# Performance work log

Measured on AMD Instinct MI355X. Metric: run time of the kernel, lower is better.

The kernel has to match this reference:

```python
import jax, jax.numpy as jnp
import numpy as np

P = 20000          # plan nodes (queries)
H = 128            # hidden_dim_plan
DIMS = {"table": (100000, 96), "pred": (400000, 160), "agg": (60000, 64), "join": (80000, 64)}
BN_EPS = 1e-5


def setup_inputs() -> dict:
    key = jax.random.key(0)
    ks = iter(jax.random.split(key, 32))
    inp = {}
    for t, (n, d) in DIMS.items():
        inp[f"feat_{t}"] = jax.random.normal(next(ks), (n, d), dtype=jnp.float32)
        inp[f"idx_{t}"] = jax.random.randint(next(ks), (n,), 0, P)
        # per-type encoder: Linear(d, H) (stored as [d, H])
        inp[f"W_{t}"] = jax.random.normal(next(ks), (d, H), dtype=jnp.float32) * 0.02
        inp[f"b_{t}"] = jnp.zeros((H,), jnp.float32)
    # est head: BatchNorm1d(4H) -> Linear(4H,H)+ReLU -> Linear(H,H)+ReLU -> Linear(H,1)
    inp["bn_gamma"] = jnp.ones((4 * H,), jnp.float32)
    inp["bn_beta"] = jnp.zeros((4 * H,), jnp.float32)
    inp["W1"] = jax.random.normal(next(ks), (4 * H, H), dtype=jnp.float32) * 0.02
    inp["b1"] = jnp.zeros((H,), jnp.float32)
    inp["W2"] = jax.random.normal(next(ks), (H, H), dtype=jnp.float32) * 0.02
    inp["b2"] = jnp.zeros((H,), jnp.float32)
    inp["W3"] = jax.random.normal(next(ks), (H, 1), dtype=jnp.float32) * 0.02
    inp["b3"] = jnp.zeros((1,), jnp.float32)
    inp["num_plan"] = P
    return inp


def _seg_mean(x, idx, num_seg):
    # DGL mean pooling: mean over incoming edges, 0 for nodes with no edges
    s = jax.ops.segment_sum(x, idx, num_segments=num_seg)
    c = jax.ops.segment_sum(jnp.ones((x.shape[0], 1), x.dtype), idx, num_segments=num_seg)
    return s / jnp.maximum(c, 1.0)


def _forward(feats, idxs, params, num_plan):
    pooled = []
    for t in ("table", "pred", "agg", "join"):
        enc = jax.nn.relu(feats[t] @ params[f"W_{t}"] + params[f"b_{t}"])  # [N_t, H]
        pooled.append(_seg_mean(enc, idxs[t], num_plan))                    # [P, H]
    x = jnp.concatenate(pooled, axis=1)  # [P, 4H]
    # BatchNorm1d (training mode: batch statistics, biased variance)
    mu = jnp.mean(x, axis=0)
    var = jnp.mean(jnp.square(x - mu), axis=0)
    x = (x - mu) * jax.lax.rsqrt(var + BN_EPS) * params["bn_gamma"] + params["bn_beta"]
    x = jax.nn.relu(x @ params["W1"] + params["b1"])
    x = jax.nn.relu(x @ params["W2"] + params["b2"])
    return x @ params["W3"] + params["b3"]  # [P, 1]


def reference(feat_table, feat_pred, feat_agg, feat_join,
              W_table, b_table, W_pred, b_pred, W_agg, b_agg, W_join, b_join,
              bn_gamma, bn_beta, W1, b1, W2, b2, W3, b3,
              idx_table, idx_pred, idx_agg, idx_join, num_plan):
    feats = {"table": feat_table, "pred": feat_pred, "agg": feat_agg, "join": feat_join}
    idxs = {"table": idx_table, "pred": idx_pred, "agg": idx_agg, "join": idx_join}
    params = dict(W_table=W_table, b_table=b_table, W_pred=W_pred, b_pred=b_pred,
                  W_agg=W_agg, b_agg=b_agg, W_join=W_join, b_join=b_join,
                  bn_gamma=bn_gamma, bn_beta=bn_beta, W1=W1, b1=b1, W2=W2, b2=b2, W3=W3, b3=b3)
    return _forward(feats, idxs, params, num_plan)
```

## Files before the change

### kernel.cpp

```cpp
#include <hip/hip_runtime.h>
#include <cstdint>


constexpr int P_N = 20000;
constexpr int HD  = 128;

typedef __attribute__((ext_vector_type(8))) short  short8v;
typedef __attribute__((ext_vector_type(4))) float  float4v;
typedef __attribute__((ext_vector_type(8))) float  float8v;
typedef __attribute__((ext_vector_type(8))) __bf16 bf16x8;

__device__ inline ushort f2bf(float f) {
    uint32_t u = __builtin_bit_cast(uint32_t, f);
    u += 0x7fffu + ((u >> 16) & 1u);
    return (ushort)(u >> 16);
}
__device__ inline short8v cvt8v(float4 a, float4 b) {
    float8v f = {a.x, a.y, a.z, a.w, b.x, b.y, b.z, b.w};
    bf16x8 h = __builtin_convertvector(f, bf16x8);
    return __builtin_bit_cast(short8v, h);
}
__device__ inline float4v mfma16(short8v a, short8v b, float4v c) {
    return __builtin_amdgcn_mfma_f32_16x16x32_bf16(a, b, c, 0, 0, 0);
}

__global__ void k_count_all(const int* __restrict__ i0, const int* __restrict__ i1,
                            const int* __restrict__ i2, const int* __restrict__ i3,
                            int n0, int n1, int n2, int n3, int* __restrict__ counts) {
    int i = blockIdx.x * blockDim.x + threadIdx.x;
    const int n01 = n0 + n1, n012 = n0 + n1 + n2, tot = n012 + n3;
    if (i >= tot) return;
    int tp, li; const int* p;
    if (i < n0)        { tp = 0; li = i;        p = i0; }
    else if (i < n01)  { tp = 1; li = i - n0;   p = i1; }
    else if (i < n012) { tp = 2; li = i - n01;  p = i2; }
    else               { tp = 3; li = i - n012; p = i3; }
    atomicAdd(&counts[tp * P_N + p[li]], 1);
}

__global__ void k_scan(int* __restrict__ counts_all, int* __restrict__ off_all,
                       int* __restrict__ cur_all, float* __restrict__ invc,
                       int* l0, int* l1, int* l2, int* l3,
                       int* s0, int* s1, int* s2, int* s3,
                       int n0, int n1, int n2, int n3) {
    const int type = blockIdx.x;
    int* counts = counts_all + type * P_N;
    int* offs   = off_all   + type * P_N;
    int* curs   = cur_all   + type * P_N;
    float* ic   = invc      + type * P_N;
    const int T = 256;
    const int CH = (P_N + T - 1) / T;
    int t = threadIdx.x;
    __shared__ int sums[T];
    __shared__ int pref[T];
    int local = 0;
    int p0 = t * CH;
    for (int i = 0; i < CH; ++i) {
        int p = p0 + i;
        if (p < P_N) local += counts[p];
    }
    sums[t] = local;
    __syncthreads();
    if (t == 0) {
        int run = 0;
        for (int j = 0; j < T; ++j) { pref[j] = run; run += sums[j]; }
    }
    __syncthreads();
    int run = pref[t];
    for (int i = 0; i < CH; ++i) {
        int p = p0 + i;
        if (p < P_N) {
            int c = counts[p];
            offs[p] = run; curs[p] = run; run += c;
            ic[p] = 1.f / (float)max(c, 1);
        }
    }
    int N; int *lp, *sp;
    if (type == 0)      { N = n0; lp = l0; sp = s0; }
    else if (type == 1) { N = n1; lp = l1; sp = s1; }
    else if (type == 2) { N = n2; lp = l2; sp = s2; }
    else                { N = n3; lp = l3; sp = s3; }
    if (t < 160) { lp[N + t] = 0; sp[N + t] = -1; }
}

__global__ void k_fill_all(const int* __restrict__ i0, const int* __restrict__ i1,
                           const int* __restrict__ i2, const int* __restrict__ i3,
                           int n0, int n1, int n2, int n3, int* __restrict__ cur_all,
                           int* l0, int* l1, int* l2, int* l3,
                           int* s0, int* s1, int* s2, int* s3) {
    int i = blockIdx.x * blockDim.x + threadIdx.x;
    const int n01 = n0 + n1, n012 = n0 + n1 + n2, tot = n012 + n3;
    if (i >= tot) return;
    int tp, li; const int* p; int *lst, *spl;
    if (i < n0)        { tp = 0; li = i;        p = i0; lst = l0; spl = s0; }
    else if (i < n01)  { tp = 1; li = i - n0;   p = i1; lst = l1; spl = s1; }
    else if (i < n012) { tp = 2; li = i - n01;  p = i2; lst = l2; spl = s2; }
    else               { tp = 3; li = i - n012; p = i3; lst = l3; spl = s3; }
    int pl = p[li];
    int pos = atomicAdd(&cur_all[tp * P_N + pl], 1);
    lst[pos] = li;
    spl[pos] = pl;
}

__global__ void k_prepw_all(const float* s0, const float* s1, const float* s2,
                            const float* s3, const float* s4, const float* s5,
                            ushort* d0, ushort* d1, ushort* d2, ushort* d3,
                            ushort* d4, ushort* d5) {
    int i = blockIdx.x * blockDim.x + threadIdx.x;
    const float* s; ushort* d; int Dv, li;
    if (i < 12288)       { s = s0; d = d0; Dv = 96;  li = i; }
    else if (i < 32768)  { s = s1; d = d1; Dv = 160; li = i - 12288; }
    else if (i < 40960)  { s = s2; d = d2; Dv = 64;  li = i - 32768; }
    else if (i < 49152)  { s = s3; d = d3; Dv = 64;  li = i - 40960; }
    else if (i < 114688) { s = s4; d = d4; Dv = 512; li = i - 49152; }
    else if (i < 131072) { s = s5; d = d5; Dv = 128; li = i - 114688; }
    else return;
    int n = li / Dv, k = li - n * Dv;
    d[li] = f2bf(s[k * HD + n]);
}

__device__ __forceinline__ void reduce_group(float (*Cs)[132], const int* plans,
                                             float* __restrict__ x, int toff, int pbase) {
    const int t = threadIdx.x;
    const int col = t & 127, half = t >> 7;
    int curp = -2; float s = 0.f;
    #pragma unroll 8
    for (int r = 0; r < 32; ++r) {
        int p = plans[pbase + half * 32 + r];
        float v = Cs[half * 32 + r][col];
        if (p != curp) {
            if (curp >= 0) atomicAdd(&x[(size_t)curp * 512 + toff + col], s);
            s = 0.f; curp = p;
        }
        if (p >= 0) s += v;
    }
    if (curp >= 0) atomicAdd(&x[(size_t)curp * 512 + toff + col], s);
}

template<int D>
__device__ __forceinline__ void enc_body(
    const float* __restrict__ feat, const ushort* __restrict__ WT,
    const float* __restrict__ bias, const int* __restrict__ list,
    const int* __restrict__ splan, float* __restrict__ x, int toff, int tile,
    float (*Cs)[132], int* plans)
{
    constexpr int NKS = D / 32;
    const int t = threadIdx.x;
    const int w = t >> 6, lane = t & 63;
    const int lq = lane >> 4, lr = lane & 15;
    const int m0 = tile * 128;

    if (t < 128) plans[t] = splan[m0 + t];
    const int l0v = list[m0 + w * 16 + lr];
    const int l1v = list[m0 + 64 + w * 16 + lr];

    const float* a0p = feat + (size_t)l0v * D + lq * 8;
    const float* a1p = feat + (size_t)l1v * D + lq * 8;

    float4 s0[2 * NKS], s1[2 * NKS];
    #pragma unroll
    for (int ks = 0; ks < NKS; ++ks) {
        s0[2 * ks]     = *(const float4*)(a0p + ks * 32);
        s0[2 * ks + 1] = *(const float4*)(a0p + ks * 32 + 4);
    }
    #pragma unroll
    for (int ks = 0; ks < NKS; ++ks) {
        s1[2 * ks]     = *(const float4*)(a1p + ks * 32);
        s1[2 * ks + 1] = *(const float4*)(a1p + ks * 32 + 4);
    }
    short8v a0[NKS], a1[NKS];
    #pragma unroll
    for (int ks = 0; ks < NKS; ++ks) a0[ks] = cvt8v(s0[2 * ks], s0[2 * ks + 1]);
    #pragma unroll
    for (int ks = 0; ks < NKS; ++ks) a1[ks] = cvt8v(s1[2 * ks], s1[2 * ks + 1]);

    float bv[8];
    #pragma unroll
    for (int nf = 0; nf < 8; ++nf) bv[nf] = bias[nf * 16 + lr];

    float4v acc0[8], acc1[8];
    #pragma unroll
    for (int nf = 0; nf < 8; ++nf) {
        acc0[nf] = (float4v){0.f, 0.f, 0.f, 0.f};
        acc1[nf] = (float4v){0.f, 0.f, 0.f, 0.f};
    }

    const ushort* wp = WT + lr * D + lq * 8;
    short8v bcur[8];
    #pragma unroll
    for (int nf = 0; nf < 8; ++nf) bcur[nf] = *(const short8v*)(wp + nf * 16 * D);
    #pragma unroll
    for (int ks = 0; ks < NKS; ++ks) {
        short8v bnxt[8];
        if (ks + 1 < NKS) {
            #pragma unroll
            for (int nf = 0; nf < 8; ++nf)
                bnxt[nf] = *(const short8v*)(wp + nf * 16 * D + (ks + 1) * 32);
        }
        #pragma unroll
        for (int nf = 0; nf < 8; ++nf) acc0[nf] = mfma16(a0[ks], bcur[nf], acc0[nf]);
        #pragma unroll
        for (int nf = 0; nf < 8; ++nf) acc1[nf] = mfma16(a1[ks], bcur[nf], acc1[nf]);
        if (ks + 1 < NKS) {
            #pragma unroll
            for (int nf = 0; nf < 8; ++nf) bcur[nf] = bnxt[nf];
        }
    }

    #pragma unroll
    for (int nf = 0; nf < 8; ++nf) {
        #pragma unroll
        for (int j = 0; j < 4; ++j)
            Cs[w * 16 + lq * 4 + j][nf * 16 + lr] = fmaxf(acc0[nf][j] + bv[nf], 0.f);
    }
    __syncthreads();
    reduce_group(Cs, plans, x, toff, 0);
    __syncthreads();
    #pragma unroll
    for (int nf = 0; nf < 8; ++nf) {
        #pragma unroll
        for (int j = 0; j < 4; ++j)
            Cs[w * 16 + lq * 4 + j][nf * 16 + lr] = fmaxf(acc1[nf][j] + bv[nf], 0.f);
    }
    __syncthreads();
    reduce_group(Cs, plans, x, toff, 64);
}

__global__ __launch_bounds__(256, 2) void k_enc_all(
    const float* f0, const float* f1, const float* f2, const float* f3,
    const ushort* w0, const ushort* w1, const ushort* w2, const ushort* w3,
    const float* b0, const float* b1, const float* b2, const float* b3,
    const int* l0, const int* l1, const int* l2, const int* l3,
    const int* s0, const int* s1, const int* s2, const int* s3,
    float* x, int ntp, int ntt, int nta)
{
    __shared__ float Cs[64][132];
    __shared__ int plans[128];
    int bid = blockIdx.x;
    if (bid < ntp) { enc_body<160>(f1, w1, b1, l1, s1, x, 128, bid, Cs, plans); return; }
    bid -= ntp;
    if (bid < ntt) { enc_body<96>(f0, w0, b0, l0, s0, x, 0, bid, Cs, plans); return; }
    bid -= ntt;
    if (bid < nta) { enc_body<64>(f2, w2, b2, l2, s2, x, 256, bid, Cs, plans); return; }
    bid -= nta;
    enc_body<64>(f3, w3, b3, l3, s3, x, 384, bid, Cs, plans);
}

__global__ __launch_bounds__(512) void k_bnstats(const float* __restrict__ x,
                                                 const float* __restrict__ invc,
                                                 float* __restrict__ bnsum) {
    const int t = threadIdx.x;
    const int r0 = blockIdx.x * 40;
    const int r1 = min(r0 + 40, P_N);
    const float* ic = invc + (t >> 7) * P_N;
    float s = 0.f, q = 0.f;
    for (int r = r0; r < r1; ++r) {
        float v = x[(size_t)r * 512 + t] * ic[r];
        s += v; q += v * v;
    }
    atomicAdd(&bnsum[t], s);
    atomicAdd(&bnsum[512 + t], q);
}

__global__ __launch_bounds__(512) void k_bnfinal(const float* __restrict__ bnsum,
                                                 const float* __restrict__ gamma, const float* __restrict__ beta,
                                                 float* __restrict__ scale, float* __restrict__ shiftv) {
    const int t = threadIdx.x;
    const float invn = 1.f / (float)P_N;
    float mu  = bnsum[t] * invn;
    float var = bnsum[512 + t] * invn - mu * mu;
    float rstd = rsqrtf(fmaxf(var, 0.f) + 1e-5f);
    float sc = gamma[t] * rstd;
    scale[t]  = sc;
    shiftv[t] = beta[t] - mu * sc;
}

__global__ __launch_bounds__(256) void k_head(
    const float* __restrict__ x, const float* __restrict__ invc,
    const float* __restrict__ scale, const float* __restrict__ shiftv,
    const ushort* __restrict__ WT1, const float* __restrict__ b1,
    const ushort* __restrict__ WT2, const float* __restrict__ b2,
    const float* __restrict__ W3, const float* __restrict__ b3,
    float* __restrict__ out)
{
    __shared__ float h[2][16][132];
    __shared__ float red[2][32];
    const int t = threadIdx.x;
    const int w = t >> 6, lane = t & 63;
    const int lq = lane >> 4, lr = lane & 15;
    const int wr = w >> 1, wc = w & 1;
    const int p0 = blockIdx.x * 32;
    const int row = p0 + wr * 16 + lr;
    const float* xr = x + (size_t)row * 512;

    float4v acc[4];
    #pragma unroll
    for (int nf = 0; nf < 4; ++nf) acc[nf] = (float4v){0.f, 0.f, 0.f, 0.f};

    #pragma unroll
    for (int kc = 0; kc < 4; ++kc) {
        const float ic = invc[kc * P_N + row];
        float4 st[8];
        #pragma unroll
        for (int k2 = 0; k2 < 4; ++k2) {
            const int k0 = kc * 128 + k2 * 32 + lq * 8;
            st[2 * k2]     = *(const float4*)(xr + k0);
            st[2 * k2 + 1] = *(const float4*)(xr + k0 + 4);
        }
        short8v a[4];
        #pragma unroll
        for (int k2 = 0; k2 < 4; ++k2) {
            const int k0 = kc * 128 + k2 * 32 + lq * 8;
            float4 sc0 = *(const float4*)(scale + k0);
            float4 sc1 = *(const float4*)(scale + k0 + 4);
            float4 sh0 = *(const float4*)(shiftv + k0);
            float4 sh1 = *(const float4*)(shiftv + k0 + 4);
            float4 v0, v1;
            v0.x = st[2*k2].x   * ic * sc0.x + sh0.x;
            v0.y = st[2*k2].y   * ic * sc0.y + sh0.y;
            v0.z = st[2*k2].z   * ic * sc0.z + sh0.z;
            v0.w = st[2*k2].w   * ic * sc0.w + sh0.w;
            v1.x = st[2*k2+1].x * ic * sc1.x + sh1.x;
            v1.y = st[2*k2+1].y * ic * sc1.y + sh1.y;
            v1.z = st[2*k2+1].z * ic * sc1.z + sh1.z;
            v1.w = st[2*k2+1].w * ic * sc1.w + sh1.w;
            a[k2] = cvt8v(v0, v1);
        }
        #pragma unroll
        for (int k2 = 0; k2 < 4; ++k2) {
            const int ks = kc * 4 + k2;
            #pragma unroll
            for (int nf = 0; nf < 4; ++nf) {
                short8v b = *(const short8v*)(WT1 + (size_t)(wc * 64 + nf * 16 + lr) * 512 + ks * 32 + lq * 8);
                acc[nf] = mfma16(a[k2], b, acc[nf]);
            }
        }
    }
    #pragma unroll
    for (int nf = 0; nf < 4; ++nf) {
        const int c = wc * 64 + nf * 16 + lr;
        const float bvv = b1[c];
        #pragma unroll
        for (int j = 0; j < 4; ++j)
            h[wr][lq * 4 + j][c] = fmaxf(acc[nf][j] + bvv, 0.f);
    }
    __syncthreads();

    short8v a2[4];
    #pragma unroll
    for (int ks = 0; ks < 4; ++ks) {
        const float* hp = &h[wr][lr][ks * 32 + lq * 8];
        a2[ks] = cvt8v(*(const float4*)hp, *(const float4*)(hp + 4));
    }
    float4v acc2[4];
    #pragma unroll
    for (int nf = 0; nf < 4; ++nf) acc2[nf] = (float4v){0.f, 0.f, 0.f, 0.f};
    #pragma unroll
    for (int ks = 0; ks < 4; ++ks) {
        #pragma unroll
        for (int nf = 0; nf < 4; ++nf) {
            short8v b = *(const short8v*)(WT2 + (wc * 64 + nf * 16 + lr) * 128 + ks * 32 + lq * 8);
            acc2[nf] = mfma16(a2[ks], b, acc2[nf]);
        }
    }

    float s0 = 0.f, s1 = 0.f, s2 = 0.f, s3 = 0.f;
    #pragma unroll
    for (int nf = 0; nf < 4; ++nf) {
        const int c = wc * 64 + nf * 16 + lr;
        const float w3v = W3[c];
        const float bvv = b2[c];
        s0 += fmaxf(acc2[nf][0] + bvv, 0.f) * w3v;
        s1 += fmaxf(acc2[nf][1] + bvv, 0.f) * w3v;
        s2 += fmaxf(acc2[nf][2] + bvv, 0.f) * w3v;
        s3 += fmaxf(acc2[nf][3] + bvv, 0.f) * w3v;
    }
    #pragma unroll
    for (int o = 1; o < 16; o <<= 1) {
        s0 += __shfl_xor(s0, o);
        s1 += __shfl_xor(s1, o);
        s2 += __shfl_xor(s2, o);
        s3 += __shfl_xor(s3, o);
    }
    if (lr == 0) {
        red[wc][wr * 16 + lq * 4 + 0] = s0;
        red[wc][wr * 16 + lq * 4 + 1] = s1;
        red[wc][wr * 16 + lq * 4 + 2] = s2;
        red[wc][wr * 16 + lq * 4 + 3] = s3;
    }
    __syncthreads();
    if (t < 32) out[p0 + t] = red[0][t] + red[1][t] + b3[0];
}

extern "C" void kernel_launch(void* const* d_in, const int* in_sizes, int n_in,
                              void* d_out, int out_size, void* d_ws, size_t ws_size,
                              hipStream_t stream)
{
    const float* feats[4] = {(const float*)d_in[0], (const float*)d_in[4], (const float*)d_in[8],  (const float*)d_in[12]};
    const int*   idxs[4]  = {(const int*)d_in[1],   (const int*)d_in[5],   (const int*)d_in[9],   (const int*)d_in[13]};
    const float* Ws[4]    = {(const float*)d_in[2], (const float*)d_in[6], (const float*)d_in[10], (const float*)d_in[14]};
    const float* bs[4]    = {(const float*)d_in[3], (const float*)d_in[7], (const float*)d_in[11], (const float*)d_in[15]};
    const float* gamma = (const float*)d_in[16];
    const float* beta  = (const float*)d_in[17];
    const float* W1 = (const float*)d_in[18]; const float* b1 = (const float*)d_in[19];
    const float* W2 = (const float*)d_in[20]; const float* b2 = (const float*)d_in[21];
    const float* W3 = (const float*)d_in[22]; const float* b3 = (const float*)d_in[23];
    int Ns[4] = {in_sizes[1], in_sizes[5], in_sizes[9], in_sizes[13]};

    char* ws = (char*)d_ws;
    int* counts = (int*)(ws + 0);
    int* offs   = (int*)(ws + 320000);
    int* curs   = (int*)(ws + 640000);
    int* lists[4];
    lists[0] = (int*)(ws + 960000);
    lists[1] = (int*)(ws + 1360640);
    lists[2] = (int*)(ws + 2961280);
    lists[3] = (int*)(ws + 3201920);
    int* splans[4];
    splans[0] = (int*)(ws + 3522560);
    splans[1] = (int*)(ws + 3923200);
    splans[2] = (int*)(ws + 5523840);
    splans[3] = (int*)(ws + 5764480);
    ushort* WTs[4];
    WTs[0] = (ushort*)(ws + 6085120);
    WTs[1] = (ushort*)(ws + 6109696);
    WTs[2] = (ushort*)(ws + 6150656);
    WTs[3] = (ushort*)(ws + 6167040);
    float* invc   = (float*)(ws + 6183424);
    float* x      = (float*)(ws + 6503424);
    float* bnsum  = (float*)(ws + 47463424);
    float* scale  = (float*)(ws + 47467520);
    float* shiftv = (float*)(ws + 47469568);
    ushort* WT1   = (ushort*)(ws + 640000);
    ushort* WT2   = (ushort*)(ws + 771072);

    hipMemsetAsync(counts, 0, 4 * P_N * sizeof(int), stream);
    hipMemsetAsync(bnsum, 0, 1024 * sizeof(float), stream);
    hipMemsetAsync(x, 0, (size_t)P_N * 512 * sizeof(float), stream);

    const int tot = Ns[0] + Ns[1] + Ns[2] + Ns[3];
    k_count_all<<<(tot + 255) / 256, 256, 0, stream>>>(
        idxs[0], idxs[1], idxs[2], idxs[3], Ns[0], Ns[1], Ns[2], Ns[3], counts);
    k_scan<<<4, 256, 0, stream>>>(counts, offs, curs, invc,
        lists[0], lists[1], lists[2], lists[3],
        splans[0], splans[1], splans[2], splans[3],
        Ns[0], Ns[1], Ns[2], Ns[3]);
    k_fill_all<<<(tot + 255) / 256, 256, 0, stream>>>(
        idxs[0], idxs[1], idxs[2], idxs[3], Ns[0], Ns[1], Ns[2], Ns[3], curs,
        lists[0], lists[1], lists[2], lists[3],
        splans[0], splans[1], splans[2], splans[3]);
    k_prepw_all<<<512, 256, 0, stream>>>(Ws[0], Ws[1], Ws[2], Ws[3], W1, W2,
        WTs[0], WTs[1], WTs[2], WTs[3], WT1, WT2);

    const int ntp = (Ns[1] + 127) / 128, ntt = (Ns[0] + 127) / 128;
    const int nta = (Ns[2] + 127) / 128, ntj = (Ns[3] + 127) / 128;
    k_enc_all<<<ntp + ntt + nta + ntj, 256, 0, stream>>>(
        feats[0], feats[1], feats[2], feats[3],
        WTs[0], WTs[1], WTs[2], WTs[3],
        bs[0], bs[1], bs[2], bs[3],
        lists[0], lists[1], lists[2], lists[3],
        splans[0], splans[1], splans[2], splans[3],
        x, ntp, ntt, nta);

    k_bnstats<<<500, 512, 0, stream>>>(x, invc, bnsum);
    k_bnfinal<<<1, 512, 0, stream>>>(bnsum, gamma, beta, scale, shiftv);
    k_head<<<P_N / 32, 256, 0, stream>>>(x, invc, scale, shiftv,
                                         WT1, b1, WT2, b2, W3, b3, (float*)d_out);
}
```

Measured before the change: 381.9 us.

## Split gather into separate bf16 pre-gather kernel and shrink encoder tiles to 64 rows

Adds a k_gather pass that reads feature rows in plan-sorted order, converts them to bf16 and writes them into a contiguous workspace buffer. The encoder kernel then loads bf16 rows directly, handles 64 rows per block instead of 128, and its launch bound is raised to 4 blocks per CU. The aim is to take the scattered fp32 gather and conversion off the MFMA kernel and raise occupancy. The cost is an extra kernel launch and an extra round trip of roughly 100MB of bf16 data through global memory, plus more atomics per output column with smaller tiles.

```diff
diff --git a/kernel.cpp b/kernel.cpp
--- a/kernel.cpp
+++ b/kernel.cpp
@@ -119,15 +119,42 @@
     d[li] = f2bf(s[k * HD + n]);
 }
 
-__device__ __forceinline__ void reduce_group(float (*Cs)[132], const int* plans,
-                                             float* __restrict__ x, int toff, int pbase) {
+template<int D>
+__device__ __forceinline__ void gather_one(const float* __restrict__ feat,
+                                           const int* __restrict__ list,
+                                           ushort* __restrict__ gfeat, int li) {
+    constexpr int UPR = D / 8;
+    int m = li / UPR;
+    int u = li - m * UPR;
+    int r = list[m];
+    const float4* s = (const float4*)(feat + (size_t)r * D + u * 8);
+    float4 x0 = s[0], x1 = s[1];
+    *(short8v*)(gfeat + (size_t)m * D + u * 8) = cvt8v(x0, x1);
+}
+
+__global__ void k_gather(const float* f0, const float* f1, const float* f2, const float* f3,
+                         const int* l0, const int* l1, const int* l2, const int* l3,
+                         ushort* g0, ushort* g1, ushort* g2, ushort* g3,
+                         int U1, int U0, int U2, int U3) {
+    int i = blockIdx.x * blockDim.x + threadIdx.x;
+    if (i < U1) { gather_one<160>(f1, l1, g1, i); return; }
+    i -= U1;
+    if (i < U0) { gather_one< 96>(f0, l0, g0, i); return; }
+    i -= U0;
+    if (i < U2) { gather_one< 64>(f2, l2, g2, i); return; }
+    i -= U2;
+    if (i < U3) { gather_one< 64>(f3, l3, g3, i); return; }
+}
+
+__device__ __forceinline__ void reduce64(float (*Cs)[132], const int* plans,
+                                         float* __restrict__ x, int toff) {
     const int t = threadIdx.x;
     const int col = t & 127, half = t >> 7;
     int curp = -2; float s = 0.f;
     #pragma unroll 8
-    for (int r = 0; r < 32; ++r) {
-        int p = plans[pbase + half * 32 + r];
-        float v = Cs[half * 32 + r][col];
+    for (int r = half * 32; r < half * 32 + 32; ++r) {
+        int p = plans[r];
+        float v = Cs[r][col];
         if (p != curp) {
             if (curp >= 0) atomicAdd(&x[(size_t)curp * 512 + toff + col], s);
             s = 0.f; curp = p;
@@ -139,51 +166,31 @@
 
 template<int D>
 __device__ __forceinline__ void enc_body(
-    const float* __restrict__ feat, const ushort* __restrict__ WT,
-    const float* __restrict__ bias, const int* __restrict__ list,
-    const int* __restrict__ splan, float* __restrict__ x, int toff, int tile,
+    const ushort* __restrict__ gfeat, const ushort* __restrict__ WT,
+    const float* __restrict__ bias, const int* __restrict__ splan,
+    float* __restrict__ x, int toff, int tile, int N,
     float (*Cs)[132], int* plans)
 {
     constexpr int NKS = D / 32;
     const int t = threadIdx.x;
     const int w = t >> 6, lane = t & 63;
     const int lq = lane >> 4, lr = lane & 15;
-    const int m0 = tile * 128;
-
-    if (t < 128) plans[t] = splan[m0 + t];
-    const int l0v = list[m0 + w * 16 + lr];
-    const int l1v = list[m0 + 64 + w * 16 + lr];
-
-    const float* a0p = feat + (size_t)l0v * D + lq * 8;
-    const float* a1p = feat + (size_t)l1v * D + lq * 8;
-
-    float4 s0[2 * NKS], s1[2 * NKS];
-    #pragma unroll
-    for (int ks = 0; ks < NKS; ++ks) {
-        s0[2 * ks]     = *(const float4*)(a0p + ks * 32);
-        s0[2 * ks + 1] = *(const float4*)(a0p + ks * 32 + 4);
-    }
-    #pragma unroll
-    for (int ks = 0; ks < NKS; ++ks) {
-        s1[2 * ks]     = *(const float4*)(a1p + ks * 32);
-        s1[2 * ks + 1] = *(const float4*)(a1p + ks * 32 + 4);
-    }
-    short8v a0[NKS], a1[NKS];
-    #pragma unroll
-    for (int ks = 0; ks < NKS; ++ks) a0[ks] = cvt8v(s0[2 * ks], s0[2 * ks + 1]);
-    #pragma unroll
-    for (int ks = 0; ks < NKS; ++ks) a1[ks] = cvt8v(s1[2 * ks], s1[2 * ks + 1]);
+    const int m0 = tile * 64;
+    if (t < 64) plans[t] = splan[m0 + t];
+
+    const int row = min(m0 + w * 16 + lr, N - 1);
+    const ushort* ap = gfeat + (size_t)row * D + lq * 8;
+    short8v a[NKS];
+    #pragma unroll
+    for (int ks = 0; ks < NKS; ++ks) a[ks] = *(const short8v*)(ap + ks * 32);
 
     float bv[8];
     #pragma unroll
     for (int nf = 0; nf < 8; ++nf) bv[nf] = bias[nf * 16 + lr];
 
-    float4v acc0[8], acc1[8];
-    #pragma unroll
-    for (int nf = 0; nf < 8; ++nf) {
-        acc0[nf] = (float4v){0.f, 0.f, 0.f, 0.f};
-        acc1[nf] = (float4v){0.f, 0.f, 0.f, 0.f};
-    }
+    float4v acc[8];
+    #pragma unroll
+    for (int nf = 0; nf < 8; ++nf) acc[nf] = (float4v){0.f, 0.f, 0.f, 0.f};
 
     const ushort* wp = WT + lr * D + lq * 8;
     short8v bcur[8];
@@ -198,9 +205,7 @@
                 bnxt[nf] = *(const short8v*)(wp + nf * 16 * D + (ks + 1) * 32);
         }
         #pragma unroll
-        for (int nf = 0; nf < 8; ++nf) acc0[nf] = mfma16(a0[ks], bcur[nf], acc0[nf]);
-        #pragma unroll
-        for (int nf = 0; nf < 8; ++nf) acc1[nf] = mfma16(a1[ks], bcur[nf], acc1[nf]);
+        for (int nf = 0; nf < 8; ++nf) acc[nf] = mfma16(a[ks], bcur[nf], acc[nf]);
         if (ks + 1 < NKS) {
             #pragma unroll
             for (int nf = 0; nf < 8; ++nf) bcur[nf] = bnxt[nf];
@@ -211,39 +216,30 @@
     for (int nf = 0; nf < 8; ++nf) {
         #pragma unroll
         for (int j = 0; j < 4; ++j)
-            Cs[w * 16 + lq * 4 + j][nf * 16 + lr] = fmaxf(acc0[nf][j] + bv[nf], 0.f);
+            Cs[w * 16 + lq * 4 + j][nf * 16 + lr] = fmaxf(acc[nf][j] + bv[nf], 0.f);
     }
     __syncthreads();
-    reduce_group(Cs, plans, x, toff, 0);
-    __syncthreads();
-    #pragma unroll
-    for (int nf = 0; nf < 8; ++nf) {
-        #pragma unroll
-        for (int j = 0; j < 4; ++j)
-            Cs[w * 16 + lq * 4 + j][nf * 16 + lr] = fmaxf(acc1[nf][j] + bv[nf], 0.f);
-    }
-    __syncthreads();
-    reduce_group(Cs, plans, x, toff, 64);
-}
-
-__global__ __launch_bounds__(256, 2) void k_enc_all(
-    const float* f0, const float* f1, const float* f2, const float* f3,
+    reduce64(Cs, plans, x, toff);
+}
+
+__global__ __launch_bounds__(256, 4) void k_enc_all(
+    const ushort* g0, const ushort* g1, const ushort* g2, const ushort* g3,
     const ushort* w0, const ushort* w1, const ushort* w2, const ushort* w3,
     const float* b0, const float* b1, const float* b2, const float* b3,
-    const int* l0, const int* l1, const int* l2, const int* l3,
     const int* s0, const int* s1, const int* s2, const int* s3,
+    int n0, int n1, int n2, int n3,
     float* x, int ntp, int ntt, int nta)
 {
     __shared__ float Cs[64][132];
-    __shared__ int plans[128];
+    __shared__ int plans[64];
     int bid = blockIdx.x;
-    if (bid < ntp) { enc_body<160>(f1, w1, b1, l1, s1, x, 128, bid, Cs, plans); return; }
+    if (bid < ntp) { enc_body<160>(g1, w1, b1, s1, x, 128, bid, n1, Cs, plans); return; }
     bid -= ntp;
-    if (bid < ntt) { enc_body<96>(f0, w0, b0, l0, s0, x, 0, bid, Cs, plans); return; }
+    if (bid < ntt) { enc_body< 96>(g0, w0, b0, s0, x, 0,   bid, n0, Cs, plans); return; }
     bid -= ntt;
-    if (bid < nta) { enc_body<64>(f2, w2, b2, l2, s2, x, 256, bid, Cs, plans); return; }
+    if (bid < nta) { enc_body< 64>(g2, w2, b2, s2, x, 256, bid, n2, Cs, plans); return; }
     bid -= nta;
-    enc_body<64>(f3, w3, b3, l3, s3, x, 384, bid, Cs, plans);
+    enc_body<64>(g3, w3, b3, s3, x, 384, bid, n3, Cs, plans);
 }
 
 __global__ __launch_bounds__(512) void k_bnstats(const float* __restrict__ x,
@@ -406,6 +402,7 @@
     const float* W2 = (const float*)d_in[20]; const float* b2 = (const float*)d_in[21];
     const float* W3 = (const float*)d_in[22]; const float* b3 = (const float*)d_in[23];
     int Ns[4] = {in_sizes[1], in_sizes[5], in_sizes[9], in_sizes[13]};
+    const int Ds[4] = {96, 160, 64, 64};
 
     char* ws = (char*)d_ws;
     int* counts = (int*)(ws + 0);
@@ -433,6 +430,10 @@
     float* shiftv = (float*)(ws + 47469568);
     ushort* WT1   = (ushort*)(ws + 640000);
     ushort* WT2   = (ushort*)(ws + 771072);
+    ushort* g0 = (ushort*)(ws + 47472640);
+    ushort* g1 = (ushort*)(ws + 66672640);
+    ushort* g2 = (ushort*)(ws + 194672640);
+    ushort* g3 = (ushort*)(ws + 202352640);
 
     hipMemsetAsync(counts, 0, 4 * P_N * sizeof(int), stream);
     hipMemsetAsync(bnsum, 0, 1024 * sizeof(float), stream);
@@ -452,14 +453,22 @@
     k_prepw_all<<<512, 256, 0, stream>>>(Ws[0], Ws[1], Ws[2], Ws[3], W1, W2,
         WTs[0], WTs[1], WTs[2], WTs[3], WT1, WT2);
 
-    const int ntp = (Ns[1] + 127) / 128, ntt = (Ns[0] + 127) / 128;
-    const int nta = (Ns[2] + 127) / 128, ntj = (Ns[3] + 127) / 128;
+    const int U0 = Ns[0] * (Ds[0] / 8), U1 = Ns[1] * (Ds[1] / 8);
+    const int U2 = Ns[2] * (Ds[2] / 8), U3 = Ns[3] * (Ds[3] / 8);
+    const int Uall = U0 + U1 + U2 + U3;
+    k_gather<<<(Uall + 255) / 256, 256, 0, stream>>>(
+        feats[0], feats[1], feats[2], feats[3],
+        lists[0], lists[1], lists[2], lists[3],
+        g0, g1, g2, g3, U1, U0, U2, U3);
+
+    const int ntp = (Ns[1] + 63) / 64, ntt = (Ns[0] + 63) / 64;
+    const int nta = (Ns[2] + 63) / 64, ntj = (Ns[3] + 63) / 64;
     k_enc_all<<<ntp + ntt + nta + ntj, 256, 0, stream>>>(
-        feats[0], feats[1], feats[2], feats[3],
+        g0, g1, g2, g3,
         WTs[0], WTs[1], WTs[2], WTs[3],
         bs[0], bs[1], bs[2], bs[3],
-        lists[0], lists[1], lists[2], lists[3],
         splans[0], splans[1], splans[2], splans[3],
+        Ns[0], Ns[1], Ns[2], Ns[3],
         x, ntp, ntt, nta);
 
     k_bnstats<<<500, 512, 0, stream>>>(x, invc, bnsum);
```

After: 454.8 us. 1.19x slower.

## Make encoder wave-independent with register-level segment reduction, drop LDS staging

Applied to the files above, without the earlier changes.

The encoder kernel now gives each wavefront its own 16-row tile instead of a 128-row block tile split into two halves. Each lane reduces its four MFMA output rows in registers using the sorted plan ids and issues atomics directly. This removes the shared-memory staging, the block barriers, and the second accumulator set, which frees registers and allows higher occupancy (launch bounds raised to 4). The cost is more global atomics, because runs are merged over only 4 rows instead of 32, and the weights are reloaded by every wave without software prefetch.

```diff
diff --git a/kernel.cpp b/kernel.cpp
--- a/kernel.cpp
+++ b/kernel.cpp
@@ -119,131 +119,85 @@
     d[li] = f2bf(s[k * HD + n]);
 }
 
-__device__ __forceinline__ void reduce_group(float (*Cs)[132], const int* plans,
-                                             float* __restrict__ x, int toff, int pbase) {
-    const int t = threadIdx.x;
-    const int col = t & 127, half = t >> 7;
-    int curp = -2; float s = 0.f;
-    #pragma unroll 8
-    for (int r = 0; r < 32; ++r) {
-        int p = plans[pbase + half * 32 + r];
-        float v = Cs[half * 32 + r][col];
-        if (p != curp) {
-            if (curp >= 0) atomicAdd(&x[(size_t)curp * 512 + toff + col], s);
-            s = 0.f; curp = p;
-        }
-        if (p >= 0) s += v;
-    }
-    if (curp >= 0) atomicAdd(&x[(size_t)curp * 512 + toff + col], s);
-}
-
 template<int D>
-__device__ __forceinline__ void enc_body(
+__device__ __forceinline__ void enc_wave(
     const float* __restrict__ feat, const ushort* __restrict__ WT,
     const float* __restrict__ bias, const int* __restrict__ list,
-    const int* __restrict__ splan, float* __restrict__ x, int toff, int tile,
-    float (*Cs)[132], int* plans)
+    const int* __restrict__ splan, float* __restrict__ x, int toff, int wtile)
 {
     constexpr int NKS = D / 32;
-    const int t = threadIdx.x;
-    const int w = t >> 6, lane = t & 63;
+    const int lane = threadIdx.x & 63;
     const int lq = lane >> 4, lr = lane & 15;
-    const int m0 = tile * 128;
-
-    if (t < 128) plans[t] = splan[m0 + t];
-    const int l0v = list[m0 + w * 16 + lr];
-    const int l1v = list[m0 + 64 + w * 16 + lr];
-
-    const float* a0p = feat + (size_t)l0v * D + lq * 8;
-    const float* a1p = feat + (size_t)l1v * D + lq * 8;
-
-    float4 s0[2 * NKS], s1[2 * NKS];
+    const int m0 = wtile * 16;
+
+    int pl0 = splan[m0 + lq * 4 + 0];
+    int pl1 = splan[m0 + lq * 4 + 1];
+    int pl2 = splan[m0 + lq * 4 + 2];
+    int pl3 = splan[m0 + lq * 4 + 3];
+
+    const int row = list[m0 + lr];
+    const float* ap = feat + (size_t)row * D + lq * 8;
+    float4 st[2 * NKS];
     #pragma unroll
     for (int ks = 0; ks < NKS; ++ks) {
-        s0[2 * ks]     = *(const float4*)(a0p + ks * 32);
-        s0[2 * ks + 1] = *(const float4*)(a0p + ks * 32 + 4);
-    }
+        st[2 * ks]     = *(const float4*)(ap + ks * 32);
+        st[2 * ks + 1] = *(const float4*)(ap + ks * 32 + 4);
+    }
+    float bv[8];
+    #pragma unroll
+    for (int nf = 0; nf < 8; ++nf) bv[nf] = bias[nf * 16 + lr];
+
+    short8v a[NKS];
+    #pragma unroll
+    for (int ks = 0; ks < NKS; ++ks) a[ks] = cvt8v(st[2 * ks], st[2 * ks + 1]);
+
+    float4v acc[8];
+    #pragma unroll
+    for (int nf = 0; nf < 8; ++nf) acc[nf] = (float4v){0.f, 0.f, 0.f, 0.f};
+
+    const ushort* wp = WT + lr * D + lq * 8;
     #pragma unroll
     for (int ks = 0; ks < NKS; ++ks) {
-        s1[2 * ks]     = *(const float4*)(a1p + ks * 32);
-        s1[2 * ks + 1] = *(const float4*)(a1p + ks * 32 + 4);
-    }
-    short8v a0[NKS], a1[NKS];
-    #pragma unroll
-    for (int ks = 0; ks < NKS; ++ks) a0[ks] = cvt8v(s0[2 * ks], s0[2 * ks + 1]);
-    #pragma unroll
-    for (int ks = 0; ks < NKS; ++ks) a1[ks] = cvt8v(s1[2 * ks], s1[2 * ks + 1]);
-
-    float bv[8];
-    #pragma unroll
-    for (int nf = 0; nf < 8; ++nf) bv[nf] = bias[nf * 16 + lr];
-
-    float4v acc0[8], acc1[8];
+        #pragma unroll
+        for (int nf = 0; nf < 8; ++nf)
+            acc[nf] = mfma16(a[ks], *(const short8v*)(wp + nf * 16 * D + ks * 32), acc[nf]);
+    }
+
+    float* xc = x + toff + lr;
     #pragma unroll
     for (int nf = 0; nf < 8; ++nf) {
-        acc0[nf] = (float4v){0.f, 0.f, 0.f, 0.f};
-        acc1[nf] = (float4v){0.f, 0.f, 0.f, 0.f};
-    }
-
-    const ushort* wp = WT + lr * D + lq * 8;
-    short8v bcur[8];
-    #pragma unroll
-    for (int nf = 0; nf < 8; ++nf) bcur[nf] = *(const short8v*)(wp + nf * 16 * D);
-    #pragma unroll
-    for (int ks = 0; ks < NKS; ++ks) {
-        short8v bnxt[8];
-        if (ks + 1 < NKS) {
-            #pragma unroll
-            for (int nf = 0; nf < 8; ++nf)
-                bnxt[nf] = *(const short8v*)(wp + nf * 16 * D + (ks + 1) * 32);
-        }
-        #pragma unroll
-        for (int nf = 0; nf < 8; ++nf) acc0[nf] = mfma16(a0[ks], bcur[nf], acc0[nf]);
-        #pragma unroll
-        for (int nf = 0; nf < 8; ++nf) acc1[nf] = mfma16(a1[ks], bcur[nf], acc1[nf]);
-        if (ks + 1 < NKS) {
-            #pragma unroll
-            for (int nf = 0; nf < 8; ++nf) bcur[nf] = bnxt[nf];
-        }
-    }
-
-    #pragma unroll
-    for (int nf = 0; nf < 8; ++nf) {
-        #pragma unroll
-        for (int j = 0; j < 4; ++j)
-            Cs[w * 16 + lq * 4 + j][nf * 16 + lr] = fmaxf(acc0[nf][j] + bv[nf], 0.f);
-    }
-    __syncthreads();
-    reduce_group(Cs, plans, x, toff, 0);
-    __syncthreads();
-    #pragma unroll
-    for (int nf = 0; nf < 8; ++nf) {
-        #pragma unroll
-        for (int j = 0; j < 4; ++j)
-            Cs[w * 16 + lq * 4 + j][nf * 16 + lr] = fmaxf(acc1[nf][j] + bv[nf], 0.f);
-    }
-    __syncthreads();
-    reduce_group(Cs, plans, x, toff, 64);
-}
-
-__global__ __launch_bounds__(256, 2) void k_enc_all(
+        float* xn = xc + nf * 16;
+        float v0 = fmaxf(acc[nf][0] + bv[nf], 0.f);
+        float v1 = fmaxf(acc[nf][1] + bv[nf], 0.f);
+        float v2 = fmaxf(acc[nf][2] + bv[nf], 0.f);
+        float v3 = fmaxf(acc[nf][3] + bv[nf], 0.f);
+        int cur = pl0; float s = v0;
+        if (pl1 != cur) { if (cur >= 0) atomicAdd(&xn[(size_t)cur * 512], s); s = 0.f; cur = pl1; }
+        s += v1;
+        if (pl2 != cur) { if (cur >= 0) atomicAdd(&xn[(size_t)cur * 512], s); s = 0.f; cur = pl2; }
+        s += v2;
+        if (pl3 != cur) { if (cur >= 0) atomicAdd(&xn[(size_t)cur * 512], s); s = 0.f; cur = pl3; }
+        s += v3;
+        if (cur >= 0) atomicAdd(&xn[(size_t)cur * 512], s);
+    }
+}
+
+__global__ __launch_bounds__(256, 4) void k_enc_all(
     const float* f0, const float* f1, const float* f2, const float* f3,
     const ushort* w0, const ushort* w1, const ushort* w2, const ushort* w3,
     const float* b0, const float* b1, const float* b2, const float* b3,
     const int* l0, const int* l1, const int* l2, const int* l3,
     const int* s0, const int* s1, const int* s2, const int* s3,
-    float* x, int ntp, int ntt, int nta)
+    float* x, int nwp, int nwt, int nwa, int nwj)
 {
-    __shared__ float Cs[64][132];
-    __shared__ int plans[128];
-    int bid = blockIdx.x;
-    if (bid < ntp) { enc_body<160>(f1, w1, b1, l1, s1, x, 128, bid, Cs, plans); return; }
-    bid -= ntp;
-    if (bid < ntt) { enc_body<96>(f0, w0, b0, l0, s0, x, 0, bid, Cs, plans); return; }
-    bid -= ntt;
-    if (bid < nta) { enc_body<64>(f2, w2, b2, l2, s2, x, 256, bid, Cs, plans); return; }
-    bid -= nta;
-    enc_body<64>(f3, w3, b3, l3, s3, x, 384, bid, Cs, plans);
+    int wid = blockIdx.x * 4 + (threadIdx.x >> 6);
+    if (wid < nwp) { enc_wave<160>(f1, w1, b1, l1, s1, x, 128, wid); return; }
+    wid -= nwp;
+    if (wid < nwt) { enc_wave< 96>(f0, w0, b0, l0, s0, x, 0,   wid); return; }
+    wid -= nwt;
+    if (wid < nwa) { enc_wave< 64>(f2, w2, b2, l2, s2, x, 256, wid); return; }
+    wid -= nwa;
+    if (wid < nwj) { enc_wave< 64>(f3, w3, b3, l3, s3, x, 384, wid); return; }
 }
 
 __global__ __launch_bounds__(512) void k_bnstats(const float* __restrict__ x,
@@ -452,15 +406,16 @@
     k_prepw_all<<<512, 256, 0, stream>>>(Ws[0], Ws[1], Ws[2], Ws[3], W1, W2,
         WTs[0], WTs[1], WTs[2], WTs[3], WT1, WT2);
 
-    const int ntp = (Ns[1] + 127) / 128, ntt = (Ns[0] + 127) / 128;
-    const int nta = (Ns[2] + 127) / 128, ntj = (Ns[3] + 127) / 128;
-    k_enc_all<<<ntp + ntt + nta + ntj, 256, 0, stream>>>(
+    const int nwp = (Ns[1] + 15) / 16, nwt = (Ns[0] + 15) / 16;
+    const int nwa = (Ns[2] + 15) / 16, nwj = (Ns[3] + 15) / 16;
+    const int nwaves = nwp + nwt + nwa + nwj;
+    k_enc_all<<<(nwaves + 3) / 4, 256, 0, stream>>>(
         feats[0], feats[1], feats[2], feats[3],
         WTs[0], WTs[1], WTs[2], WTs[3],
         bs[0], bs[1], bs[2], bs[3],
         lists[0], lists[1], lists[2], lists[3],
         splans[0], splans[1], splans[2], splans[3],
-        x, ntp, ntt, nta);
+        x, nwp, nwt, nwa, nwj);
 
     k_bnstats<<<500, 512, 0, stream>>>(x, invc, bnsum);
     k_bnfinal<<<1, 512, 0, stream>>>(bnsum, gamma, beta, scale, shiftv);
```

New measurement: 470.9 us. 1.23x slower.
